# Performance work log

Hardware: AMD Instinct MI355X
Metric: run time of the kernel (lower is better)

The kernel has to match this reference:

```python
import jax, jax.numpy as jnp
import numpy as np

B, S, D, H = 16, 512, 1024, 16
DH = D // H  # 64


def setup_inputs() -> dict:
    key = jax.random.key(0)
    kx, kq, kk, kv = jax.random.split(key, 4)
    stdv = 1.0 / np.sqrt(DH)  # reset_param uses 1/sqrt(t.size(1)) = 1/sqrt(head_dim)
    x = jax.random.normal(kx, (B, S, D), dtype=jnp.float32)
    Wq = jax.random.uniform(kq, (H, D, DH), dtype=jnp.float32, minval=-stdv, maxval=stdv)
    Wk = jax.random.uniform(kk, (H, D, DH), dtype=jnp.float32, minval=-stdv, maxval=stdv)
    Wv = jax.random.uniform(kv, (H, D, DH), dtype=jnp.float32, minval=-stdv, maxval=stdv)
    return {"x": x, "Wq": Wq, "Wk": Wk, "Wv": Wv}


def reference(x, Wq, Wk, Wv):
    # x: [B, S, D]; Wq/Wk/Wv: [H, D, DH] (stacked per-head params)
    q = jnp.einsum('bsd,hde->bhse', x, Wq)  # [B,H,S,DH]
    k = jnp.einsum('bsd,hde->bhse', x, Wk)
    v = jnp.einsum('bsd,hde->bhse', x, Wv)
    # NOTE: original scales by sqrt(input_dim), not sqrt(head_dim)
    scale = 1.0 / jnp.sqrt(jnp.float32(D))
    scores = jnp.einsum('bhse,bhte->bhst', q, k) * scale  # [B,H,S,S]
    attn = jax.nn.softmax(scores, axis=-1)
    out = jnp.einsum('bhst,bhte->bhse', attn, v)  # [B,H,S,DH]
    # concat heads along feature dim (head order matches torch cat over loop)
    return out.transpose(0, 2, 1, 3).reshape(x.shape[0], x.shape[1], D)
```

## Files before the change

### kernel.cpp

```cpp
#include <hip/hip_runtime.h>
#include <math.h>

constexpr int B = 16, S = 512, D = 1024, H = 16, DH = 64;
constexpr int BH = B * H;

typedef short bf16x8 __attribute__((ext_vector_type(8)));
typedef float f32x4  __attribute__((ext_vector_type(4)));

__device__ __forceinline__ unsigned short f2bf(float f) {
    unsigned u = __float_as_uint(f);
    u += 0x7fff + ((u >> 16) & 1);
    return (unsigned short)(u >> 16);
}

__global__ __launch_bounds__(256) void convert_x(
    const float* __restrict__ x, unsigned short* __restrict__ xb)
{
    int i = blockIdx.x * 256 + threadIdx.x;
    float4 v = ((const float4*)x)[i];
    ushort4 o;
    o.x = f2bf(v.x); o.y = f2bf(v.y); o.z = f2bf(v.z); o.w = f2bf(v.w);
    ((ushort4*)xb)[i] = o;
}

__global__ __launch_bounds__(256) void convert_w(
    const float* __restrict__ Wq, const float* __restrict__ Wk,
    const float* __restrict__ Wv, unsigned short* __restrict__ WbT)
{
    __shared__ float tile[64][65];
    const int d0 = blockIdx.x * 64;
    const int h = blockIdx.y, m = blockIdx.z;
    const float* W = ((m == 0) ? Wq : (m == 1) ? Wk : Wv) + (size_t)h * D * DH;
    const int t = threadIdx.x;
    {
        int e = t & 63, dr = t >> 6;
        #pragma unroll
        for (int i = 0; i < 16; ++i) {
            int d = dr * 16 + i;
            tile[d][e] = W[(size_t)(d0 + d) * DH + e];
        }
    }
    __syncthreads();
    {
        int d = t & 63, er = t >> 6;
        unsigned short* out = WbT + (size_t)(m * H + h) * DH * D;
        #pragma unroll
        for (int i = 0; i < 16; ++i) {
            int e = er * 16 + i;
            out[(size_t)e * D + d0 + d] = f2bf(tile[d][e]);
        }
    }
}

__global__ __launch_bounds__(256) void qkv_gemm(
    const unsigned short* __restrict__ xb,
    const unsigned short* __restrict__ WbT,
    unsigned short* __restrict__ qkvb)
{
    __shared__ unsigned short As[128 * 64];
    __shared__ unsigned short Bs[128 * 64];

    const int t = threadIdx.x;
    const int w = t >> 6;
    const int wr = w >> 1, wc = w & 1;
    const int L = t & 63;
    const int lane15 = L & 15;
    const int quad = L >> 4;
    const int lrow8 = L >> 3;
    const int lg = L & 7;

    const int r0 = blockIdx.x * 128;
    const int n0 = blockIdx.y * 128;

    f32x4 acc[4][4] = {};

    for (int k0 = 0; k0 < D; k0 += 64) {
        #pragma unroll
        for (int i = 0; i < 4; ++i) {
            int c = w * 4 + i;
            int r = c * 8 + lrow8;
            int gg = lg ^ (r & 7);
            const unsigned short* gp = xb + (size_t)(r0 + r) * D + k0 + gg * 8;
            __builtin_amdgcn_global_load_lds(
                (const __attribute__((address_space(1))) void*)gp,
                (__attribute__((address_space(3))) void*)(As + c * 512),
                16, 0, 0);
            const unsigned short* gq = WbT + (size_t)(n0 + r) * D + k0 + gg * 8;
            __builtin_amdgcn_global_load_lds(
                (const __attribute__((address_space(1))) void*)gq,
                (__attribute__((address_space(3))) void*)(Bs + c * 512),
                16, 0, 0);
        }
        __syncthreads();

        #pragma unroll
        for (int ks = 0; ks < 2; ++ks) {
            int gk = ks * 4 + quad;
            bf16x8 a[4], bb[4];
            #pragma unroll
            for (int rt = 0; rt < 4; ++rt) {
                int ml = wr * 64 + rt * 16 + lane15;
                a[rt] = *(const bf16x8*)(As + ml * 64 + ((gk ^ (ml & 7)) * 8));
            }
            #pragma unroll
            for (int ct = 0; ct < 4; ++ct) {
                int nl = wc * 64 + ct * 16 + lane15;
                bb[ct] = *(const bf16x8*)(Bs + nl * 64 + ((gk ^ (nl & 7)) * 8));
            }
            #pragma unroll
            for (int rt = 0; rt < 4; ++rt)
                #pragma unroll
                for (int ct = 0; ct < 4; ++ct)
                    acc[rt][ct] = __builtin_amdgcn_mfma_f32_16x16x32_bf16(
                        a[rt], bb[ct], acc[rt][ct], 0, 0, 0);
        }
        __syncthreads();
    }

    const int m  = n0 >> 10;
    const int h  = ((n0 >> 6) + wc) & 15;
    const int bb_ = r0 >> 9;
    const int s0 = (r0 & 511) + wr * 64;

    if (m == 2) {
        unsigned short* outv = qkvb + ((size_t)(2 * BH) + (bb_ * H + h)) * (size_t)(S * DH);
        #pragma unroll
        for (int rt = 0; rt < 4; ++rt) {
            int srow = s0 + rt * 16 + quad * 4;
            #pragma unroll
            for (int ct = 0; ct < 4; ++ct) {
                int e = ct * 16 + lane15;
                ushort4 pk;
                pk.x = f2bf(acc[rt][ct][0]);
                pk.y = f2bf(acc[rt][ct][1]);
                pk.z = f2bf(acc[rt][ct][2]);
                pk.w = f2bf(acc[rt][ct][3]);
                *(ushort4*)(outv + (size_t)e * S + srow) = pk;
            }
        }
    } else {
        const float sc = (m == 0) ? 0.04508422002778011f : 1.0f;
        unsigned short* out = qkvb + ((size_t)m * BH + (bb_ * H + h)) * (size_t)(S * DH);
        #pragma unroll
        for (int rt = 0; rt < 4; ++rt) {
            #pragma unroll
            for (int ct = 0; ct < 4; ++ct) {
                int e = ct * 16 + lane15;
                #pragma unroll
                for (int r = 0; r < 4; ++r) {
                    int srow = s0 + rt * 16 + quad * 4 + r;
                    out[(size_t)srow * DH + e] = f2bf(acc[rt][ct][r] * sc);
                }
            }
        }
    }
}

__global__ __launch_bounds__(256) void attn_mfma(
    const unsigned short* __restrict__ qkvb, float* __restrict__ out)
{
    __shared__ unsigned short Qs[128 * 64];
    __shared__ unsigned short Ks[64 * 64];
    __shared__ unsigned short Vt[64 * 64];
    __shared__ unsigned short Ps[4 * 32 * 64];

    const int t = threadIdx.x;
    const int w = t >> 6;
    const int L = t & 63;
    const int lane15 = L & 15;
    const int quad = L >> 4;
    const int lrow8 = L >> 3;
    const int lg = L & 7;
    const int qr0 = blockIdx.x * 128;
    const int bh = blockIdx.y;
    const int b = bh >> 4, h = bh & 15;

    const unsigned short* qb = qkvb + (size_t)bh * S * DH;
    const unsigned short* kb = qkvb + (size_t)(BH + bh) * S * DH;
    const unsigned short* vt = qkvb + (size_t)(2 * BH + bh) * S * DH;

    #pragma unroll
    for (int i = 0; i < 4; ++i) {
        int base = w * 32 + i * 8;
        int r = base + lrow8;
        int gg = lg ^ (r & 7);
        const unsigned short* gp = qb + (size_t)(qr0 + r) * DH + gg * 8;
        __builtin_amdgcn_global_load_lds(
            (const __attribute__((address_space(1))) void*)gp,
            (__attribute__((address_space(3))) void*)(Qs + base * 64),
            16, 0, 0);
    }

    f32x4 o[2][4] = {};
    float plsum[2][4] = {{0.f,0.f,0.f,0.f},{0.f,0.f,0.f,0.f}};

    bf16x8 qf[2][2];
    unsigned short* Pw = Ps + w * 2048;

    for (int kt = 0; kt < S; kt += 64) {
        #pragma unroll
        for (int i = 0; i < 2; ++i) {
            int base = (w * 2 + i) * 8;
            int r = base + lrow8;
            int gg = lg ^ (r & 7);
            const unsigned short* gpk = kb + (size_t)(kt + r) * DH + gg * 8;
            __builtin_amdgcn_global_load_lds(
                (const __attribute__((address_space(1))) void*)gpk,
                (__attribute__((address_space(3))) void*)(Ks + base * 64),
                16, 0, 0);
            const unsigned short* gpv = vt + (size_t)r * S + kt + gg * 8;
            __builtin_amdgcn_global_load_lds(
                (const __attribute__((address_space(1))) void*)gpv,
                (__attribute__((address_space(3))) void*)(Vt + base * 64),
                16, 0, 0);
        }
        __syncthreads();

        if (kt == 0) {
            #pragma unroll
            for (int mt = 0; mt < 2; ++mt)
                #pragma unroll
                for (int ks = 0; ks < 2; ++ks) {
                    int ml = w * 32 + mt * 16 + lane15;
                    int gk = ks * 4 + quad;
                    qf[mt][ks] = *(const bf16x8*)(Qs + ml * 64 + ((gk ^ (lane15 & 7)) * 8));
                }
        }

        f32x4 sc[2][4] = {};
        #pragma unroll
        for (int ks = 0; ks < 2; ++ks) {
            int gk = ks * 4 + quad;
            bf16x8 kf[4];
            #pragma unroll
            for (int ct = 0; ct < 4; ++ct) {
                int key = ct * 16 + lane15;
                kf[ct] = *(const bf16x8*)(Ks + key * 64 + ((gk ^ (lane15 & 7)) * 8));
            }
            #pragma unroll
            for (int mt = 0; mt < 2; ++mt)
                #pragma unroll
                for (int ct = 0; ct < 4; ++ct)
                    sc[mt][ct] = __builtin_amdgcn_mfma_f32_16x16x32_bf16(
                        qf[mt][ks], kf[ct], sc[mt][ct], 0, 0, 0);
        }

        #pragma unroll
        for (int mt = 0; mt < 2; ++mt) {
            #pragma unroll
            for (int reg = 0; reg < 4; ++reg) {
                int rr = mt * 16 + quad * 4 + reg;
                float p0 = exp2f(sc[mt][0][reg]);
                float p1 = exp2f(sc[mt][1][reg]);
                float p2 = exp2f(sc[mt][2][reg]);
                float p3 = exp2f(sc[mt][3][reg]);
                int sw = (rr & 7) ^ ((rr >> 3) & 1);
                int vhi = lane15 >> 3, ulo = lane15 & 7;
                unsigned short* pr = Pw + rr * 64 + ulo;
                pr[((0 + vhi) ^ sw) * 8] = f2bf(p0);
                pr[((2 + vhi) ^ sw) * 8] = f2bf(p1);
                pr[((4 + vhi) ^ sw) * 8] = f2bf(p2);
                pr[((6 + vhi) ^ sw) * 8] = f2bf(p3);
                plsum[mt][reg] += (p0 + p1) + (p2 + p3);
            }
        }

        #pragma unroll
        for (int ks = 0; ks < 2; ++ks) {
            int gk = ks * 4 + quad;
            bf16x8 pf[2], vf[4];
            #pragma unroll
            for (int mt = 0; mt < 2; ++mt) {
                int rr = mt * 16 + lane15;
                int pg = gk ^ (rr & 7) ^ ((rr >> 3) & 1);
                pf[mt] = *(const bf16x8*)(Pw + rr * 64 + pg * 8);
            }
            #pragma unroll
            for (int nt = 0; nt < 4; ++nt) {
                int dh = nt * 16 + lane15;
                vf[nt] = *(const bf16x8*)(Vt + dh * 64 + ((gk ^ (lane15 & 7)) * 8));
            }
            #pragma unroll
            for (int mt = 0; mt < 2; ++mt)
                #pragma unroll
                for (int nt = 0; nt < 4; ++nt)
                    o[mt][nt] = __builtin_amdgcn_mfma_f32_16x16x32_bf16(
                        pf[mt], vf[nt], o[mt][nt], 0, 0, 0);
        }
        __syncthreads();
    }

    #pragma unroll
    for (int mt = 0; mt < 2; ++mt) {
        #pragma unroll
        for (int reg = 0; reg < 4; ++reg) {
            float l = plsum[mt][reg];
            #pragma unroll
            for (int d = 1; d < 16; d <<= 1)
                l += __shfl_xor(l, d, 64);
            float inv = 1.0f / l;
            int srow = qr0 + w * 32 + mt * 16 + quad * 4 + reg;
            float* op = out + (size_t)(b * S + srow) * D + h * DH;
            #pragma unroll
            for (int nt = 0; nt < 4; ++nt)
                op[nt * 16 + lane15] = o[mt][nt][reg] * inv;
        }
    }
}

extern "C" void kernel_launch(void* const* d_in, const int* in_sizes, int n_in,
                              void* d_out, int out_size, void* d_ws, size_t ws_size,
                              hipStream_t stream) {
    const float* x  = (const float*)d_in[0];
    const float* Wq = (const float*)d_in[1];
    const float* Wk = (const float*)d_in[2];
    const float* Wv = (const float*)d_in[3];
    float* outp = (float*)d_out;

    unsigned short* qkvb = (unsigned short*)d_ws;
    unsigned short* xb   = (unsigned short*)((char*)d_ws + 50331648);
    unsigned short* WbT  = (unsigned short*)((char*)d_ws + 67108864);

    convert_x<<<dim3((B * S * D / 4) / 256), 256, 0, stream>>>(x, xb);
    convert_w<<<dim3(D / 64, H, 3), 256, 0, stream>>>(Wq, Wk, Wv, WbT);
    qkv_gemm<<<dim3(B * S / 128, 3 * H * DH / 128), 256, 0, stream>>>(xb, WbT, qkvb);
    attn_mfma<<<dim3(S / 128, BH), 256, 0, stream>>>(qkvb, outp);
}
```

Baseline: 201.2 us.

## Compute transposed scores so P stays in registers, dropping the LDS round-trip

Swaps the MFMA operands so each lane holds a column of the transposed score tile, then packs the exponentiated probabilities straight into B-operand registers for the PV MFMA. The per-wave P scratch buffer in shared memory and its writes and reads go away. To line the key order up with the packed P layout, the K rows are loaded in a permuted order. The output becomes column-major per lane, so the row-sum reduction now needs only two shuffles and the stores become float4 writes.

```diff
diff --git a/kernel.cpp b/kernel.cpp
--- a/kernel.cpp
+++ b/kernel.cpp
@@ -162,7 +162,6 @@
     __shared__ unsigned short Qs[128 * 64];
     __shared__ unsigned short Ks[64 * 64];
     __shared__ unsigned short Vt[64 * 64];
-    __shared__ unsigned short Ps[4 * 32 * 64];
 
     const int t = threadIdx.x;
     const int w = t >> 6;
@@ -192,18 +191,17 @@
     }
 
     f32x4 o[2][4] = {};
-    float plsum[2][4] = {{0.f,0.f,0.f,0.f},{0.f,0.f,0.f,0.f}};
-
+    float plsum[2] = {0.f, 0.f};
     bf16x8 qf[2][2];
-    unsigned short* Pw = Ps + w * 2048;
 
     for (int kt = 0; kt < S; kt += 64) {
         #pragma unroll
         for (int i = 0; i < 2; ++i) {
             int base = (w * 2 + i) * 8;
             int r = base + lrow8;
+            int gr = (r & 32) | ((r & 12) << 1) | ((r & 16) >> 2) | (r & 3);
             int gg = lg ^ (r & 7);
-            const unsigned short* gpk = kb + (size_t)(kt + r) * DH + gg * 8;
+            const unsigned short* gpk = kb + (size_t)(kt + gr) * DH + gg * 8;
             __builtin_amdgcn_global_load_lds(
                 (const __attribute__((address_space(1))) void*)gpk,
                 (__attribute__((address_space(3))) void*)(Ks + base * 64),
@@ -227,54 +225,48 @@
                 }
         }
 
-        f32x4 sc[2][4] = {};
+        f32x4 st[2][4] = {};
         #pragma unroll
         for (int ks = 0; ks < 2; ++ks) {
             int gk = ks * 4 + quad;
             bf16x8 kf[4];
             #pragma unroll
             for (int ct = 0; ct < 4; ++ct) {
-                int key = ct * 16 + lane15;
-                kf[ct] = *(const bf16x8*)(Ks + key * 64 + ((gk ^ (lane15 & 7)) * 8));
+                int kr = ct * 16 + lane15;
+                kf[ct] = *(const bf16x8*)(Ks + kr * 64 + ((gk ^ (lane15 & 7)) * 8));
             }
             #pragma unroll
             for (int mt = 0; mt < 2; ++mt)
                 #pragma unroll
                 for (int ct = 0; ct < 4; ++ct)
-                    sc[mt][ct] = __builtin_amdgcn_mfma_f32_16x16x32_bf16(
-                        qf[mt][ks], kf[ct], sc[mt][ct], 0, 0, 0);
-        }
-
+                    st[mt][ct] = __builtin_amdgcn_mfma_f32_16x16x32_bf16(
+                        kf[ct], qf[mt][ks], st[mt][ct], 0, 0, 0);
+        }
+
+        bf16x8 pB[2][2];
         #pragma unroll
         for (int mt = 0; mt < 2; ++mt) {
-            #pragma unroll
-            for (int reg = 0; reg < 4; ++reg) {
-                int rr = mt * 16 + quad * 4 + reg;
-                float p0 = exp2f(sc[mt][0][reg]);
-                float p1 = exp2f(sc[mt][1][reg]);
-                float p2 = exp2f(sc[mt][2][reg]);
-                float p3 = exp2f(sc[mt][3][reg]);
-                int sw = (rr & 7) ^ ((rr >> 3) & 1);
-                int vhi = lane15 >> 3, ulo = lane15 & 7;
-                unsigned short* pr = Pw + rr * 64 + ulo;
-                pr[((0 + vhi) ^ sw) * 8] = f2bf(p0);
-                pr[((2 + vhi) ^ sw) * 8] = f2bf(p1);
-                pr[((4 + vhi) ^ sw) * 8] = f2bf(p2);
-                pr[((6 + vhi) ^ sw) * 8] = f2bf(p3);
-                plsum[mt][reg] += (p0 + p1) + (p2 + p3);
-            }
+            float rs = 0.f;
+            #pragma unroll
+            for (int ct = 0; ct < 4; ++ct) {
+                float p0 = exp2f(st[mt][ct][0]);
+                float p1 = exp2f(st[mt][ct][1]);
+                float p2 = exp2f(st[mt][ct][2]);
+                float p3 = exp2f(st[mt][ct][3]);
+                rs += (p0 + p1) + (p2 + p3);
+                int hi = (ct & 1) * 4;
+                pB[mt][ct >> 1][hi + 0] = (short)f2bf(p0);
+                pB[mt][ct >> 1][hi + 1] = (short)f2bf(p1);
+                pB[mt][ct >> 1][hi + 2] = (short)f2bf(p2);
+                pB[mt][ct >> 1][hi + 3] = (short)f2bf(p3);
+            }
+            plsum[mt] += rs;
         }
 
         #pragma unroll
         for (int ks = 0; ks < 2; ++ks) {
             int gk = ks * 4 + quad;
-            bf16x8 pf[2], vf[4];
-            #pragma unroll
-            for (int mt = 0; mt < 2; ++mt) {
-                int rr = mt * 16 + lane15;
-                int pg = gk ^ (rr & 7) ^ ((rr >> 3) & 1);
-                pf[mt] = *(const bf16x8*)(Pw + rr * 64 + pg * 8);
-            }
+            bf16x8 vf[4];
             #pragma unroll
             for (int nt = 0; nt < 4; ++nt) {
                 int dh = nt * 16 + lane15;
@@ -285,25 +277,27 @@
                 #pragma unroll
                 for (int nt = 0; nt < 4; ++nt)
                     o[mt][nt] = __builtin_amdgcn_mfma_f32_16x16x32_bf16(
-                        pf[mt], vf[nt], o[mt][nt], 0, 0, 0);
+                        vf[nt], pB[mt][ks], o[mt][nt], 0, 0, 0);
         }
         __syncthreads();
     }
 
     #pragma unroll
     for (int mt = 0; mt < 2; ++mt) {
-        #pragma unroll
-        for (int reg = 0; reg < 4; ++reg) {
-            float l = plsum[mt][reg];
-            #pragma unroll
-            for (int d = 1; d < 16; d <<= 1)
-                l += __shfl_xor(l, d, 64);
-            float inv = 1.0f / l;
-            int srow = qr0 + w * 32 + mt * 16 + quad * 4 + reg;
-            float* op = out + (size_t)(b * S + srow) * D + h * DH;
-            #pragma unroll
-            for (int nt = 0; nt < 4; ++nt)
-                op[nt * 16 + lane15] = o[mt][nt][reg] * inv;
+        float l = plsum[mt];
+        l += __shfl_xor(l, 16, 64);
+        l += __shfl_xor(l, 32, 64);
+        float inv = 1.0f / l;
+        int srow = qr0 + w * 32 + mt * 16 + lane15;
+        float* op = out + (size_t)(b * S + srow) * D + h * DH;
+        #pragma unroll
+        for (int nt = 0; nt < 4; ++nt) {
+            float4 v;
+            v.x = o[mt][nt][0] * inv;
+            v.y = o[mt][nt][1] * inv;
+            v.z = o[mt][nt][2] * inv;
+            v.w = o[mt][nt][3] * inv;
+            *(float4*)(op + nt * 16 + quad * 4) = v;
         }
     }
 }
```

After: 194.5 us. 1.03x faster.
